# Kernel tuning notes

Measured on AMD Instinct MI355X. Metric: run time of the kernel, lower is better.

The kernel has to match this reference:

```python
import jax, jax.numpy as jnp
import numpy as np

NUM_CLASSES = 9
TEMP = 0.1
ALPHA = 0.99
EPS = 1e-12  # F.normalize default eps


def _l2norm(x, axis=-1):
    n = jnp.linalg.norm(x, axis=axis, keepdims=True)
    return x / jnp.maximum(n, EPS)


def setup_inputs() -> dict:
    key = jax.random.key(0)
    k1, k2, k3, k4, k5 = jax.random.split(key, 5)
    B, D, h, w = 4, 768, 128, 128
    return {
        "cls_score": jax.random.normal(k1, (B, NUM_CLASSES, h, w), dtype=jnp.float32),
        "label": jax.random.randint(k2, (B, 4 * h, 4 * w), 0, NUM_CLASSES, dtype=jnp.int64),
        "gt_lucas": jax.random.randint(k3, (B, 4 * h, 4 * w), 0, NUM_CLASSES, dtype=jnp.int64),
        "features": jax.random.normal(k4, (B, D, h, w), dtype=jnp.float32),
        "prototypes": jax.random.uniform(k5, (NUM_CLASSES, D), dtype=jnp.float32),
    }


def reference(cls_score, label, gt_lucas, features, prototypes):
    B, D, h, w = features.shape
    # so the masked gathers reduce to a full flatten (static shapes).
    corine = label[:, ::4, ::4].reshape(-1)          # [N]
    lucas = gt_lucas[:, ::4, ::4].reshape(-1)        # [N] (mask trivially all valid)
    feats = jnp.transpose(features, (0, 2, 3, 1)).reshape(-1, D)  # [N, D]
    N = feats.shape[0]
    # note: original indexes corine labels under the lucas mask (mask all-true here)
    labels_lucas = corine
    labels_corine = jnp.where(corine == 7, 6, corine)
    # per-class EMA prototype update (unique(labels_lucas) == arange(9) by construction;
    # compute_ema detaches the new mean)
    sums = jax.ops.segment_sum(feats, labels_lucas, num_segments=NUM_CLASSES)      # [C, D]
    counts = jax.ops.segment_sum(jnp.ones((N,), feats.dtype), labels_lucas,
                                 num_segments=NUM_CLASSES)                          # [C]
    means = jax.lax.stop_gradient(sums / counts[:, None])
    protos = ALPHA * means + (1.0 - ALPHA) * prototypes
    protos = _l2norm(protos, axis=-1)                # F.normalize over feature dim
    logits = protos @ feats.T                        # [C, N]
    prot_feat = _l2norm(logits, axis=-1) / TEMP      # normalize each class row over N
    prot_feat = prot_feat.at[2].set((labels_corine == 2).astype(prot_feat.dtype))
    E = jnp.exp(prot_feat)                           # [C, N]
    A1 = E[labels_corine, jnp.arange(N)]             # [N]
    A2 = E.sum(axis=0)                               # [N]
    return jnp.mean(-jnp.log(A1 / A2))
```

## Files before the change

### kernel.cpp

```cpp
#include <hip/hip_runtime.h>
#include <math.h>

#define NCLS 9
#define DIM 768
#define NPIX 65536

#define OFF_LAB     ((size_t)0)
#define OFF_HIST    ((size_t)65536)
#define OFF_SUMS    ((size_t)74752)
#define OFF_SUMSQ   ((size_t)102400)
#define OFF_LOSS    ((size_t)102464)
#define OFF_DONE    ((size_t)102480)
#define OFF_LOGITS  ((size_t)131072)

__device__ __forceinline__ float waveReduceSum(float v) {
#pragma unroll
  for (int off = 32; off > 0; off >>= 1) v += __shfl_down(v, off, 64);
  return v;
}

__global__ void k0_lab(const int* __restrict__ label, unsigned char* __restrict__ lab,
                       int* __restrict__ hist, float* __restrict__ sumsq,
                       float* __restrict__ lossacc, unsigned int* __restrict__ done) {
  __shared__ int h[NCLS];
  int tid = threadIdx.x;
  if (tid < NCLS) h[tid] = 0;
  __syncthreads();
  int n = blockIdx.x * 256 + tid;
  int b = n >> 14, r = (n >> 7) & 127, cc = n & 127;
  int c = label[b * 262144 + r * 2048 + cc * 4];
  lab[n] = (unsigned char)c;
  atomicAdd(&h[c], 1);
  if (blockIdx.x == 0) {
    if (tid < 16) sumsq[tid] = 0.f;
    else if (tid == 16) lossacc[0] = 0.f;
    else if (tid == 17) done[0] = 0u;
  }
  __syncthreads();
  if (tid < NCLS) hist[blockIdx.x * NCLS + tid] = h[tid];
}

__global__ void k1_segsum(const float4* __restrict__ feat4, const uchar4* __restrict__ lab4,
                          float* __restrict__ sums) {
  int d = blockIdx.x;
  int tid = threadIdx.x;
  float acc[NCLS];
#pragma unroll
  for (int k = 0; k < NCLS; ++k) acc[k] = 0.f;
  for (int b = 0; b < 4; ++b) {
    const float4* fp = feat4 + (size_t)(b * DIM + d) * 4096;
    const uchar4* lp = lab4 + b * 4096;
#pragma unroll 4
    for (int i = 0; i < 16; ++i) {
      int p = tid + i * 256;
      float4 f = fp[p];
      uchar4 l = lp[p];
      int lx = l.x, ly = l.y, lz = l.z, lw = l.w;
#pragma unroll
      for (int k = 0; k < NCLS; ++k) {
        acc[k] += (lx == k) ? f.x : 0.f;
        acc[k] += (ly == k) ? f.y : 0.f;
        acc[k] += (lz == k) ? f.z : 0.f;
        acc[k] += (lw == k) ? f.w : 0.f;
      }
    }
  }
  __shared__ float red[4][NCLS];
#pragma unroll
  for (int k = 0; k < NCLS; ++k) acc[k] = waveReduceSum(acc[k]);
  int lane = tid & 63, w = tid >> 6;
  if (lane == 0) {
#pragma unroll
    for (int k = 0; k < NCLS; ++k) red[w][k] = acc[k];
  }
  __syncthreads();
  if (tid < NCLS)
    sums[tid * DIM + d] = red[0][tid] + red[1][tid] + red[2][tid] + red[3][tid];
}

__global__ void __launch_bounds__(1024) k3_fused(const float* __restrict__ sums,
                                                 const int* __restrict__ hist,
                                                 const float* __restrict__ proto,
                                                 const float* __restrict__ feat,
                                                 float* __restrict__ logits,
                                                 float* __restrict__ sumsq) {
  __shared__ float pl[DIM * 12];
  __shared__ float cpart[32][NCLS];
  __shared__ float cnt[NCLS];
  __shared__ float red12[12][NCLS];
  __shared__ float invn[NCLS];
  __shared__ float red4[4][NCLS];
  int tid = threadIdx.x;

  if (tid < 288) {
    int c = tid % NCLS, g = tid / NCLS;
    int s = 0;
#pragma unroll
    for (int j = 0; j < 8; ++j) s += hist[(g * 8 + j) * NCLS + c];
    cpart[g][c] = (float)s;
  }
  __syncthreads();
  if (tid < NCLS) {
    float s = 0.f;
#pragma unroll
    for (int g = 0; g < 32; ++g) s += cpart[g][tid];
    cnt[tid] = s;
  }
  __syncthreads();

  float v[NCLS];
  if (tid < DIM) {
#pragma unroll
    for (int c = 0; c < NCLS; ++c)
      v[c] = 0.99f * (sums[c * DIM + tid] / cnt[c]) + 0.01f * proto[c * DIM + tid];
    int lane = tid & 63, w = tid >> 6;
#pragma unroll
    for (int c = 0; c < NCLS; ++c) {
      float q = waveReduceSum(v[c] * v[c]);
      if (lane == 0) red12[w][c] = q;
    }
  }
  __syncthreads();
  if (tid < NCLS) {
    float t = 0.f;
#pragma unroll
    for (int w2 = 0; w2 < 12; ++w2) t += red12[w2][tid];
    invn[tid] = 1.f / fmaxf(sqrtf(t), 1e-12f);
  }
  __syncthreads();
  if (tid < DIM) {
#pragma unroll
    for (int c = 0; c < NCLS; ++c) pl[tid * 12 + c] = v[c] * invn[c];
  }
  __syncthreads();

  int s = tid >> 8, p = tid & 255;
  int n = blockIdx.x * 256 + p;
  int b = n >> 14, pp = n & 16383;
  const float* fp = feat + ((size_t)(b * DIM + s * 192)) * 16384 + pp;
  const float* plbase = pl + (size_t)s * 192 * 12;
  float a0 = 0, a1 = 0, a2 = 0, a3 = 0, a4 = 0, a5 = 0, a6 = 0, a7 = 0, a8 = 0;
#pragma unroll 4
  for (int dd = 0; dd < 192; ++dd) {
    float f = fp[(size_t)dd * 16384];
    const float4* pr = (const float4*)(plbase + dd * 12);
    float4 q0 = pr[0];
    float4 q1 = pr[1];
    float q8 = plbase[dd * 12 + 8];
    a0 += q0.x * f; a1 += q0.y * f; a2 += q0.z * f; a3 += q0.w * f;
    a4 += q1.x * f; a5 += q1.y * f; a6 += q1.z * f; a7 += q1.w * f;
    a8 += q8 * f;
  }
  __syncthreads();
  if (s > 0) {
    float* rp = pl + (size_t)(s - 1) * 2304 + p * 9;
    rp[0] = a0; rp[1] = a1; rp[2] = a2; rp[3] = a3; rp[4] = a4;
    rp[5] = a5; rp[6] = a6; rp[7] = a7; rp[8] = a8;
  }
  __syncthreads();
  if (s == 0) {
#pragma unroll
    for (int q = 0; q < 3; ++q) {
      const float* rp = pl + (size_t)q * 2304 + p * 9;
      a0 += rp[0]; a1 += rp[1]; a2 += rp[2]; a3 += rp[3]; a4 += rp[4];
      a5 += rp[5]; a6 += rp[6]; a7 += rp[7]; a8 += rp[8];
    }
    float* outp = logits + n;
    outp[0 * NPIX] = a0; outp[1 * NPIX] = a1; outp[2 * NPIX] = a2;
    outp[3 * NPIX] = a3; outp[4 * NPIX] = a4; outp[5 * NPIX] = a5;
    outp[6 * NPIX] = a6; outp[7 * NPIX] = a7; outp[8 * NPIX] = a8;
    float ss[NCLS] = {a0 * a0, a1 * a1, a2 * a2, a3 * a3, a4 * a4,
                      a5 * a5, a6 * a6, a7 * a7, a8 * a8};
#pragma unroll
    for (int c = 0; c < NCLS; ++c) ss[c] = waveReduceSum(ss[c]);
    int lane = tid & 63, w = tid >> 6;
    if (lane == 0) {
#pragma unroll
      for (int c = 0; c < NCLS; ++c) red4[w][c] = ss[c];
    }
  }
  __syncthreads();
  if (tid < NCLS)
    atomicAdd(&sumsq[tid], red4[0][tid] + red4[1][tid] + red4[2][tid] + red4[3][tid]);
}

__global__ void k5_loss(const float4* __restrict__ logits4, const uchar4* __restrict__ lab4,
                        const float* __restrict__ sumsq, float* __restrict__ lossacc,
                        unsigned int* __restrict__ done, float* __restrict__ out) {
  int t = blockIdx.x * 256 + threadIdx.x;
  int tid = threadIdx.x;
  float scale[NCLS];
#pragma unroll
  for (int c = 0; c < NCLS; ++c) scale[c] = 10.f / fmaxf(sqrtf(sumsq[c]), 1e-12f);
  float arr[NCLS][4];
#pragma unroll
  for (int c = 0; c < NCLS; ++c) {
    float4 v = logits4[(size_t)c * 16384 + t];
    arr[c][0] = v.x; arr[c][1] = v.y; arr[c][2] = v.z; arr[c][3] = v.w;
  }
  uchar4 lb = lab4[t];
  int lv[4] = {lb.x, lb.y, lb.z, lb.w};
  float lsum = 0.f;
#pragma unroll
  for (int j = 0; j < 4; ++j) {
    int l = lv[j];
    int lc = (l == 7) ? 6 : l;
    float sumE = 0.f, picked = 0.f;
#pragma unroll
    for (int c = 0; c < NCLS; ++c) {
      float pf = (c == 2) ? ((lc == 2) ? 1.f : 0.f) : arr[c][j] * scale[c];
      sumE += __expf(pf);
      picked += (c == lc) ? pf : 0.f;
    }
    lsum += __logf(sumE) - picked;
  }
  lsum = waveReduceSum(lsum);
  __shared__ float red[4];
  int lane = tid & 63, w = tid >> 6;
  if (lane == 0) red[w] = lsum;
  __syncthreads();
  if (tid == 0) {
    atomicAdd(lossacc, red[0] + red[1] + red[2] + red[3]);
    __threadfence();
    unsigned int ticket = atomicAdd(done, 1u);
    if (ticket == gridDim.x - 1) {
      __threadfence();
      float total = __hip_atomic_load(lossacc, __ATOMIC_ACQUIRE, __HIP_MEMORY_SCOPE_AGENT);
      out[0] = total * (1.f / (float)NPIX);
    }
  }
}

extern "C" void kernel_launch(void* const* d_in, const int* in_sizes, int n_in,
                              void* d_out, int out_size, void* d_ws, size_t ws_size,
                              hipStream_t stream) {
  const int* label = (const int*)d_in[1];
  const float* feat = (const float*)d_in[3];
  const float* proto = (const float*)d_in[4];
  char* ws = (char*)d_ws;
  unsigned char* lab = (unsigned char*)(ws + OFF_LAB);
  int* hist = (int*)(ws + OFF_HIST);
  float* sums = (float*)(ws + OFF_SUMS);
  float* sumsq = (float*)(ws + OFF_SUMSQ);
  float* lossacc = (float*)(ws + OFF_LOSS);
  unsigned int* done = (unsigned int*)(ws + OFF_DONE);
  float* logits = (float*)(ws + OFF_LOGITS);

  k0_lab<<<NPIX / 256, 256, 0, stream>>>(label, lab, hist, sumsq, lossacc, done);
  k1_segsum<<<DIM, 256, 0, stream>>>((const float4*)feat, (const uchar4*)lab, sums);
  k3_fused<<<NPIX / 256, 1024, 0, stream>>>(sums, hist, proto, feat, logits, sumsq);
  k5_loss<<<64, 256, 0, stream>>>((const float4*)logits, (const uchar4*)lab, sumsq, lossacc,
                                  done, (float*)d_out);
}
```

Measured before the change: 98.60 us.

## Move prototype normalization to last segsum block and split D across 16 waves

The prototype EMA and L2-normalization now run once, in the last-finishing block of the segment-sum kernel via a ticket counter, and the result is written to a workspace table. Before, each of the 256 logits blocks recomputed it. The logits kernel now copies that table into shared memory and splits the feature dimension across 16 waves of 48 rows each. Each lane computes 4 pixels and 9 classes, and partial sums are combined with shared-memory atomics. This cuts redundant per-block prologue work and raises per-thread reuse of the prototype loads, at the cost of a serial tail block in segsum and contention on the LDS atomics.

```diff
diff --git a/kernel.cpp b/kernel.cpp
--- a/kernel.cpp
+++ b/kernel.cpp
@@ -11,7 +11,9 @@
 #define OFF_SUMSQ   ((size_t)102400)
 #define OFF_LOSS    ((size_t)102464)
 #define OFF_DONE    ((size_t)102480)
-#define OFF_LOGITS  ((size_t)131072)
+#define OFF_DONE1   ((size_t)102496)
+#define OFF_PROTO   ((size_t)102528)
+#define OFF_LOGITS  ((size_t)139392)
 
 __device__ __forceinline__ float waveReduceSum(float v) {
 #pragma unroll
@@ -21,7 +23,8 @@
 
 __global__ void k0_lab(const int* __restrict__ label, unsigned char* __restrict__ lab,
                        int* __restrict__ hist, float* __restrict__ sumsq,
-                       float* __restrict__ lossacc, unsigned int* __restrict__ done) {
+                       float* __restrict__ lossacc, unsigned int* __restrict__ done,
+                       unsigned int* __restrict__ done1) {
   __shared__ int h[NCLS];
   int tid = threadIdx.x;
   if (tid < NCLS) h[tid] = 0;
@@ -35,13 +38,17 @@
     if (tid < 16) sumsq[tid] = 0.f;
     else if (tid == 16) lossacc[0] = 0.f;
     else if (tid == 17) done[0] = 0u;
+    else if (tid == 18) done1[0] = 0u;
   }
   __syncthreads();
   if (tid < NCLS) hist[blockIdx.x * NCLS + tid] = h[tid];
 }
 
 __global__ void k1_segsum(const float4* __restrict__ feat4, const uchar4* __restrict__ lab4,
-                          float* __restrict__ sums) {
+                          float* __restrict__ sums, const int* __restrict__ hist,
+                          const float* __restrict__ proto, float* __restrict__ protoT,
+                          unsigned int* __restrict__ done1) {
+  __shared__ float red[4][NCLS];
   int d = blockIdx.x;
   int tid = threadIdx.x;
   float acc[NCLS];
@@ -65,7 +72,6 @@
       }
     }
   }
-  __shared__ float red[4][NCLS];
 #pragma unroll
   for (int k = 0; k < NCLS; ++k) acc[k] = waveReduceSum(acc[k]);
   int lane = tid & 63, w = tid >> 6;
@@ -76,107 +82,137 @@
   __syncthreads();
   if (tid < NCLS)
     sums[tid * DIM + d] = red[0][tid] + red[1][tid] + red[2][tid] + red[3][tid];
-}
-
-__global__ void __launch_bounds__(1024) k3_fused(const float* __restrict__ sums,
-                                                 const int* __restrict__ hist,
-                                                 const float* __restrict__ proto,
-                                                 const float* __restrict__ feat,
-                                                 float* __restrict__ logits,
-                                                 float* __restrict__ sumsq) {
-  __shared__ float pl[DIM * 12];
-  __shared__ float cpart[32][NCLS];
+
+  __threadfence();
+  __syncthreads();
+  __shared__ unsigned int tkt;
+  if (tid == 0) tkt = atomicAdd(done1, 1u);
+  __syncthreads();
+  if (tkt != gridDim.x - 1) return;
+  __threadfence();
+
+  __shared__ float cpart[16][NCLS];
   __shared__ float cnt[NCLS];
-  __shared__ float red12[12][NCLS];
   __shared__ float invn[NCLS];
-  __shared__ float red4[4][NCLS];
-  int tid = threadIdx.x;
-
-  if (tid < 288) {
+  if (tid < 144) {
     int c = tid % NCLS, g = tid / NCLS;
     int s = 0;
 #pragma unroll
-    for (int j = 0; j < 8; ++j) s += hist[(g * 8 + j) * NCLS + c];
+    for (int j = 0; j < 16; ++j) s += hist[(g * 16 + j) * NCLS + c];
     cpart[g][c] = (float)s;
   }
   __syncthreads();
   if (tid < NCLS) {
     float s = 0.f;
 #pragma unroll
-    for (int g = 0; g < 32; ++g) s += cpart[g][tid];
+    for (int g = 0; g < 16; ++g) s += cpart[g][tid];
     cnt[tid] = s;
   }
   __syncthreads();
-
-  float v[NCLS];
-  if (tid < DIM) {
+  float v[3][NCLS];
+  float q[NCLS];
+#pragma unroll
+  for (int c = 0; c < NCLS; ++c) q[c] = 0.f;
+#pragma unroll
+  for (int j = 0; j < 3; ++j) {
+    int dd = tid + j * 256;
+#pragma unroll
+    for (int c = 0; c < NCLS; ++c) {
+      float x = 0.99f * (sums[c * DIM + dd] / cnt[c]) + 0.01f * proto[c * DIM + dd];
+      v[j][c] = x;
+      q[c] += x * x;
+    }
+  }
+#pragma unroll
+  for (int c = 0; c < NCLS; ++c) q[c] = waveReduceSum(q[c]);
+  if (lane == 0) {
+#pragma unroll
+    for (int c = 0; c < NCLS; ++c) red[w][c] = q[c];
+  }
+  __syncthreads();
+  if (tid < NCLS) {
+    float t = red[0][tid] + red[1][tid] + red[2][tid] + red[3][tid];
+    invn[tid] = 1.f / fmaxf(sqrtf(t), 1e-12f);
+  }
+  __syncthreads();
+#pragma unroll
+  for (int j = 0; j < 3; ++j) {
 #pragma unroll
     for (int c = 0; c < NCLS; ++c)
-      v[c] = 0.99f * (sums[c * DIM + tid] / cnt[c]) + 0.01f * proto[c * DIM + tid];
-    int lane = tid & 63, w = tid >> 6;
-#pragma unroll
-    for (int c = 0; c < NCLS; ++c) {
-      float q = waveReduceSum(v[c] * v[c]);
-      if (lane == 0) red12[w][c] = q;
-    }
-  }
-  __syncthreads();
-  if (tid < NCLS) {
-    float t = 0.f;
-#pragma unroll
-    for (int w2 = 0; w2 < 12; ++w2) t += red12[w2][tid];
-    invn[tid] = 1.f / fmaxf(sqrtf(t), 1e-12f);
-  }
-  __syncthreads();
-  if (tid < DIM) {
-#pragma unroll
-    for (int c = 0; c < NCLS; ++c) pl[tid * 12 + c] = v[c] * invn[c];
-  }
-  __syncthreads();
-
-  int s = tid >> 8, p = tid & 255;
-  int n = blockIdx.x * 256 + p;
-  int b = n >> 14, pp = n & 16383;
-  const float* fp = feat + ((size_t)(b * DIM + s * 192)) * 16384 + pp;
-  const float* plbase = pl + (size_t)s * 192 * 12;
-  float a0 = 0, a1 = 0, a2 = 0, a3 = 0, a4 = 0, a5 = 0, a6 = 0, a7 = 0, a8 = 0;
+      protoT[(size_t)(tid + j * 256) * 12 + c] = v[j][c] * invn[c];
+  }
+}
+
+__global__ void __launch_bounds__(1024) k3_logits(const float* __restrict__ feat,
+                                                  const float* __restrict__ protoT,
+                                                  float* __restrict__ logits,
+                                                  float* __restrict__ sumsq) {
+  __shared__ float pl[DIM * 12];
+  __shared__ float accb[NCLS][256];
+  __shared__ float red4[4][NCLS];
+  int tid = threadIdx.x;
+  const float4* pt4 = (const float4*)protoT;
+  float4* pl4 = (float4*)pl;
+  float* accf = (float*)accb;
+#pragma unroll
+  for (int i = 0; i < 3; ++i) {
+    int idx = tid + i * 1024;
+    if (idx < 2304) {
+      pl4[idx] = pt4[idx];
+      accf[idx] = 0.f;
+    }
+  }
+  __syncthreads();
+
+  int s = tid >> 6, lane = tid & 63;
+  int n0 = blockIdx.x * 256;
+  int b = n0 >> 14, ppb = n0 & 16383;
+  const float* fp = feat + ((size_t)(b * DIM + s * 48)) * 16384 + ppb + lane;
+  const float* plb = pl + (size_t)s * 48 * 12;
+  float a[NCLS][4];
+#pragma unroll
+  for (int c = 0; c < NCLS; ++c)
+#pragma unroll
+    for (int j = 0; j < 4; ++j) a[c][j] = 0.f;
+
 #pragma unroll 4
-  for (int dd = 0; dd < 192; ++dd) {
-    float f = fp[(size_t)dd * 16384];
-    const float4* pr = (const float4*)(plbase + dd * 12);
+  for (int dd = 0; dd < 48; ++dd) {
+    const float* fr = fp + (size_t)dd * 16384;
+    float f[4];
+    f[0] = fr[0]; f[1] = fr[64]; f[2] = fr[128]; f[3] = fr[192];
+    const float4* pr = (const float4*)(plb + dd * 12);
     float4 q0 = pr[0];
     float4 q1 = pr[1];
-    float q8 = plbase[dd * 12 + 8];
-    a0 += q0.x * f; a1 += q0.y * f; a2 += q0.z * f; a3 += q0.w * f;
-    a4 += q1.x * f; a5 += q1.y * f; a6 += q1.z * f; a7 += q1.w * f;
-    a8 += q8 * f;
-  }
-  __syncthreads();
-  if (s > 0) {
-    float* rp = pl + (size_t)(s - 1) * 2304 + p * 9;
-    rp[0] = a0; rp[1] = a1; rp[2] = a2; rp[3] = a3; rp[4] = a4;
-    rp[5] = a5; rp[6] = a6; rp[7] = a7; rp[8] = a8;
-  }
-  __syncthreads();
-  if (s == 0) {
-#pragma unroll
-    for (int q = 0; q < 3; ++q) {
-      const float* rp = pl + (size_t)q * 2304 + p * 9;
-      a0 += rp[0]; a1 += rp[1]; a2 += rp[2]; a3 += rp[3]; a4 += rp[4];
-      a5 += rp[5]; a6 += rp[6]; a7 += rp[7]; a8 += rp[8];
-    }
-    float* outp = logits + n;
-    outp[0 * NPIX] = a0; outp[1 * NPIX] = a1; outp[2 * NPIX] = a2;
-    outp[3 * NPIX] = a3; outp[4 * NPIX] = a4; outp[5 * NPIX] = a5;
-    outp[6 * NPIX] = a6; outp[7 * NPIX] = a7; outp[8 * NPIX] = a8;
-    float ss[NCLS] = {a0 * a0, a1 * a1, a2 * a2, a3 * a3, a4 * a4,
-                      a5 * a5, a6 * a6, a7 * a7, a8 * a8};
+    float q8 = plb[dd * 12 + 8];
+    float pcs[NCLS] = {q0.x, q0.y, q0.z, q0.w, q1.x, q1.y, q1.z, q1.w, q8};
+#pragma unroll
+    for (int c = 0; c < NCLS; ++c)
+#pragma unroll
+      for (int j = 0; j < 4; ++j) a[c][j] += pcs[c] * f[j];
+  }
+
+#pragma unroll
+  for (int c = 0; c < NCLS; ++c)
+#pragma unroll
+    for (int j = 0; j < 4; ++j)
+      atomicAdd(&accb[c][lane + 64 * j], a[c][j]);
+  __syncthreads();
+
+  if (tid < 256) {
+    int n = n0 + tid;
+    float ss[NCLS];
+#pragma unroll
+    for (int c = 0; c < NCLS; ++c) {
+      float vv = accb[c][tid];
+      logits[(size_t)c * NPIX + n] = vv;
+      ss[c] = vv * vv;
+    }
 #pragma unroll
     for (int c = 0; c < NCLS; ++c) ss[c] = waveReduceSum(ss[c]);
-    int lane = tid & 63, w = tid >> 6;
-    if (lane == 0) {
-#pragma unroll
-      for (int c = 0; c < NCLS; ++c) red4[w][c] = ss[c];
+    int l2 = tid & 63, w2 = tid >> 6;
+    if (l2 == 0) {
+#pragma unroll
+      for (int c = 0; c < NCLS; ++c) red4[w2][c] = ss[c];
     }
   }
   __syncthreads();
@@ -244,11 +280,14 @@
   float* sumsq = (float*)(ws + OFF_SUMSQ);
   float* lossacc = (float*)(ws + OFF_LOSS);
   unsigned int* done = (unsigned int*)(ws + OFF_DONE);
+  unsigned int* done1 = (unsigned int*)(ws + OFF_DONE1);
+  float* protoT = (float*)(ws + OFF_PROTO);
   float* logits = (float*)(ws + OFF_LOGITS);
 
-  k0_lab<<<NPIX / 256, 256, 0, stream>>>(label, lab, hist, sumsq, lossacc, done);
-  k1_segsum<<<DIM, 256, 0, stream>>>((const float4*)feat, (const uchar4*)lab, sums);
-  k3_fused<<<NPIX / 256, 1024, 0, stream>>>(sums, hist, proto, feat, logits, sumsq);
+  k0_lab<<<NPIX / 256, 256, 0, stream>>>(label, lab, hist, sumsq, lossacc, done, done1);
+  k1_segsum<<<DIM, 256, 0, stream>>>((const float4*)feat, (const uchar4*)lab, sums, hist,
+                                     proto, protoT, done1);
+  k3_logits<<<NPIX / 256, 1024, 0, stream>>>(feat, protoT, logits, sumsq);
   k5_loss<<<64, 256, 0, stream>>>((const float4*)logits, (const uchar4*)lab, sumsq, lossacc,
                                   done, (float*)d_out);
 }
```

After: 205.3 us. 2.08x slower.

## Fuse logits and loss kernels with grid-wide barrier, keep logits in registers

Applied to the files above, without the earlier changes.

Merges the projection kernel and the loss kernel into one launch. Each block publishes per-class partial sums of squares, waits at a software grid barrier (atomic counter plus spin), then reduces all partials and computes the loss straight from register-held logits. This removes the global logits buffer write and read-back and one kernel launch. The barrier only works if all 256 blocks of 1024 threads are co-resident, and spinning adds latency.

```diff
diff --git a/kernel.cpp b/kernel.cpp
--- a/kernel.cpp
+++ b/kernel.cpp
@@ -8,10 +8,9 @@
 #define OFF_LAB     ((size_t)0)
 #define OFF_HIST    ((size_t)65536)
 #define OFF_SUMS    ((size_t)74752)
-#define OFF_SUMSQ   ((size_t)102400)
-#define OFF_LOSS    ((size_t)102464)
-#define OFF_DONE    ((size_t)102480)
-#define OFF_LOGITS  ((size_t)131072)
+#define OFF_SSQP    ((size_t)102400)
+#define OFF_LOSS    ((size_t)111616)
+#define OFF_DONE    ((size_t)111632)
 
 __device__ __forceinline__ float waveReduceSum(float v) {
 #pragma unroll
@@ -20,8 +19,8 @@
 }
 
 __global__ void k0_lab(const int* __restrict__ label, unsigned char* __restrict__ lab,
-                       int* __restrict__ hist, float* __restrict__ sumsq,
-                       float* __restrict__ lossacc, unsigned int* __restrict__ done) {
+                       int* __restrict__ hist, float* __restrict__ lossacc,
+                       unsigned int* __restrict__ done) {
   __shared__ int h[NCLS];
   int tid = threadIdx.x;
   if (tid < NCLS) h[tid] = 0;
@@ -32,9 +31,9 @@
   lab[n] = (unsigned char)c;
   atomicAdd(&h[c], 1);
   if (blockIdx.x == 0) {
-    if (tid < 16) sumsq[tid] = 0.f;
-    else if (tid == 16) lossacc[0] = 0.f;
+    if (tid == 16) lossacc[0] = 0.f;
     else if (tid == 17) done[0] = 0u;
+    else if (tid == 18) done[1] = 0u;
   }
   __syncthreads();
   if (tid < NCLS) hist[blockIdx.x * NCLS + tid] = h[tid];
@@ -78,18 +77,20 @@
     sums[tid * DIM + d] = red[0][tid] + red[1][tid] + red[2][tid] + red[3][tid];
 }
 
-__global__ void __launch_bounds__(1024) k3_fused(const float* __restrict__ sums,
-                                                 const int* __restrict__ hist,
-                                                 const float* __restrict__ proto,
-                                                 const float* __restrict__ feat,
-                                                 float* __restrict__ logits,
-                                                 float* __restrict__ sumsq) {
+__global__ void __launch_bounds__(1024, 4) k3_mega(
+    const float* __restrict__ sums, const int* __restrict__ hist,
+    const float* __restrict__ proto, const float* __restrict__ feat,
+    const unsigned char* __restrict__ lab, float* __restrict__ ssqpart,
+    float* __restrict__ lossacc, unsigned int* __restrict__ done,
+    float* __restrict__ out) {
   __shared__ float pl[DIM * 12];
   __shared__ float cpart[32][NCLS];
   __shared__ float cnt[NCLS];
   __shared__ float red12[12][NCLS];
   __shared__ float invn[NCLS];
   __shared__ float red4[4][NCLS];
+  __shared__ float scale_s[NCLS];
+  __shared__ float lred[4];
   int tid = threadIdx.x;
 
   if (tid < 288) {
@@ -108,45 +109,46 @@
   }
   __syncthreads();
 
-  float v[NCLS];
-  if (tid < DIM) {
-#pragma unroll
-    for (int c = 0; c < NCLS; ++c)
-      v[c] = 0.99f * (sums[c * DIM + tid] / cnt[c]) + 0.01f * proto[c * DIM + tid];
-    int lane = tid & 63, w = tid >> 6;
-#pragma unroll
-    for (int c = 0; c < NCLS; ++c) {
-      float q = waveReduceSum(v[c] * v[c]);
-      if (lane == 0) red12[w][c] = q;
-    }
-  }
-  __syncthreads();
-  if (tid < NCLS) {
-    float t = 0.f;
-#pragma unroll
-    for (int w2 = 0; w2 < 12; ++w2) t += red12[w2][tid];
-    invn[tid] = 1.f / fmaxf(sqrtf(t), 1e-12f);
-  }
-  __syncthreads();
-  if (tid < DIM) {
-#pragma unroll
-    for (int c = 0; c < NCLS; ++c) pl[tid * 12 + c] = v[c] * invn[c];
-  }
-  __syncthreads();
+  {
+    float v[NCLS];
+    if (tid < DIM) {
+#pragma unroll
+      for (int c = 0; c < NCLS; ++c)
+        v[c] = 0.99f * (sums[c * DIM + tid] / cnt[c]) + 0.01f * proto[c * DIM + tid];
+      int lane = tid & 63, w = tid >> 6;
+#pragma unroll
+      for (int c = 0; c < NCLS; ++c) {
+        float q = waveReduceSum(v[c] * v[c]);
+        if (lane == 0) red12[w][c] = q;
+      }
+    }
+    __syncthreads();
+    if (tid < NCLS) {
+      float t = 0.f;
+#pragma unroll
+      for (int w2 = 0; w2 < 12; ++w2) t += red12[w2][tid];
+      invn[tid] = 1.f / fmaxf(sqrtf(t), 1e-12f);
+    }
+    __syncthreads();
+    if (tid < DIM) {
+#pragma unroll
+      for (int c = 0; c < NCLS; ++c) pl[tid * 12 + c] = v[c] * invn[c];
+    }
+    __syncthreads();
+  }
 
   int s = tid >> 8, p = tid & 255;
   int n = blockIdx.x * 256 + p;
   int b = n >> 14, pp = n & 16383;
   const float* fp = feat + ((size_t)(b * DIM + s * 192)) * 16384 + pp;
-  const float* plbase = pl + (size_t)s * 192 * 12;
   float a0 = 0, a1 = 0, a2 = 0, a3 = 0, a4 = 0, a5 = 0, a6 = 0, a7 = 0, a8 = 0;
 #pragma unroll 4
   for (int dd = 0; dd < 192; ++dd) {
     float f = fp[(size_t)dd * 16384];
-    const float4* pr = (const float4*)(plbase + dd * 12);
+    const float4* pr = (const float4*)&pl[(s * 192 + dd) * 12];
     float4 q0 = pr[0];
     float4 q1 = pr[1];
-    float q8 = plbase[dd * 12 + 8];
+    float q8 = pl[(s * 192 + dd) * 12 + 8];
     a0 += q0.x * f; a1 += q0.y * f; a2 += q0.z * f; a3 += q0.w * f;
     a4 += q1.x * f; a5 += q1.y * f; a6 += q1.z * f; a7 += q1.w * f;
     a8 += q8 * f;
@@ -165,10 +167,6 @@
       a0 += rp[0]; a1 += rp[1]; a2 += rp[2]; a3 += rp[3]; a4 += rp[4];
       a5 += rp[5]; a6 += rp[6]; a7 += rp[7]; a8 += rp[8];
     }
-    float* outp = logits + n;
-    outp[0 * NPIX] = a0; outp[1 * NPIX] = a1; outp[2 * NPIX] = a2;
-    outp[3 * NPIX] = a3; outp[4 * NPIX] = a4; outp[5 * NPIX] = a5;
-    outp[6 * NPIX] = a6; outp[7 * NPIX] = a7; outp[8 * NPIX] = a8;
     float ss[NCLS] = {a0 * a0, a1 * a1, a2 * a2, a3 * a3, a4 * a4,
                       a5 * a5, a6 * a6, a7 * a7, a8 * a8};
 #pragma unroll
@@ -180,49 +178,62 @@
     }
   }
   __syncthreads();
-  if (tid < NCLS)
-    atomicAdd(&sumsq[tid], red4[0][tid] + red4[1][tid] + red4[2][tid] + red4[3][tid]);
-}
-
-__global__ void k5_loss(const float4* __restrict__ logits4, const uchar4* __restrict__ lab4,
-                        const float* __restrict__ sumsq, float* __restrict__ lossacc,
-                        unsigned int* __restrict__ done, float* __restrict__ out) {
-  int t = blockIdx.x * 256 + threadIdx.x;
-  int tid = threadIdx.x;
-  float scale[NCLS];
-#pragma unroll
-  for (int c = 0; c < NCLS; ++c) scale[c] = 10.f / fmaxf(sqrtf(sumsq[c]), 1e-12f);
-  float arr[NCLS][4];
-#pragma unroll
-  for (int c = 0; c < NCLS; ++c) {
-    float4 v = logits4[(size_t)c * 16384 + t];
-    arr[c][0] = v.x; arr[c][1] = v.y; arr[c][2] = v.z; arr[c][3] = v.w;
-  }
-  uchar4 lb = lab4[t];
-  int lv[4] = {lb.x, lb.y, lb.z, lb.w};
-  float lsum = 0.f;
-#pragma unroll
-  for (int j = 0; j < 4; ++j) {
-    int l = lv[j];
+  if (tid < NCLS) {
+    float t = red4[0][tid] + red4[1][tid] + red4[2][tid] + red4[3][tid];
+    __hip_atomic_store(&ssqpart[blockIdx.x * NCLS + tid], t, __ATOMIC_RELAXED,
+                       __HIP_MEMORY_SCOPE_AGENT);
+  }
+  __syncthreads();
+
+  if (tid == 0) {
+    __threadfence();
+    atomicAdd(&done[0], 1u);
+    while (__hip_atomic_load(&done[0], __ATOMIC_ACQUIRE, __HIP_MEMORY_SCOPE_AGENT) <
+           gridDim.x) {
+      __builtin_amdgcn_s_sleep(2);
+    }
+  }
+  __syncthreads();
+
+  if (tid < 288) {
+    int c = tid % NCLS, g = tid / NCLS;
+    float t = 0.f;
+#pragma unroll
+    for (int j = 0; j < 8; ++j)
+      t += __hip_atomic_load(&ssqpart[(g * 8 + j) * NCLS + c], __ATOMIC_RELAXED,
+                             __HIP_MEMORY_SCOPE_AGENT);
+    cpart[g][c] = t;
+  }
+  __syncthreads();
+  if (tid < NCLS) {
+    float t = 0.f;
+#pragma unroll
+    for (int g = 0; g < 32; ++g) t += cpart[g][tid];
+    scale_s[tid] = 10.f / fmaxf(sqrtf(t), 1e-12f);
+  }
+  __syncthreads();
+
+  if (s == 0) {
+    int l = lab[n];
     int lc = (l == 7) ? 6 : l;
+    float av[NCLS] = {a0, a1, a2, a3, a4, a5, a6, a7, a8};
     float sumE = 0.f, picked = 0.f;
 #pragma unroll
     for (int c = 0; c < NCLS; ++c) {
-      float pf = (c == 2) ? ((lc == 2) ? 1.f : 0.f) : arr[c][j] * scale[c];
+      float pf = (c == 2) ? ((lc == 2) ? 1.f : 0.f) : av[c] * scale_s[c];
       sumE += __expf(pf);
       picked += (c == lc) ? pf : 0.f;
     }
-    lsum += __logf(sumE) - picked;
-  }
-  lsum = waveReduceSum(lsum);
-  __shared__ float red[4];
-  int lane = tid & 63, w = tid >> 6;
-  if (lane == 0) red[w] = lsum;
+    float lsum = __logf(sumE) - picked;
+    lsum = waveReduceSum(lsum);
+    int lane = tid & 63, w = tid >> 6;
+    if (lane == 0) lred[w] = lsum;
+  }
   __syncthreads();
   if (tid == 0) {
-    atomicAdd(lossacc, red[0] + red[1] + red[2] + red[3]);
+    atomicAdd(lossacc, lred[0] + lred[1] + lred[2] + lred[3]);
     __threadfence();
-    unsigned int ticket = atomicAdd(done, 1u);
+    unsigned int ticket = atomicAdd(&done[1], 1u);
     if (ticket == gridDim.x - 1) {
       __threadfence();
       float total = __hip_atomic_load(lossacc, __ATOMIC_ACQUIRE, __HIP_MEMORY_SCOPE_AGENT);
@@ -241,14 +252,12 @@
   unsigned char* lab = (unsigned char*)(ws + OFF_LAB);
   int* hist = (int*)(ws + OFF_HIST);
   float* sums = (float*)(ws + OFF_SUMS);
-  float* sumsq = (float*)(ws + OFF_SUMSQ);
+  float* ssqpart = (float*)(ws + OFF_SSQP);
   float* lossacc = (float*)(ws + OFF_LOSS);
   unsigned int* done = (unsigned int*)(ws + OFF_DONE);
-  float* logits = (float*)(ws + OFF_LOGITS);
-
-  k0_lab<<<NPIX / 256, 256, 0, stream>>>(label, lab, hist, sumsq, lossacc, done);
+
+  k0_lab<<<NPIX / 256, 256, 0, stream>>>(label, lab, hist, lossacc, done);
   k1_segsum<<<DIM, 256, 0, stream>>>((const float4*)feat, (const uchar4*)lab, sums);
-  k3_fused<<<NPIX / 256, 1024, 0, stream>>>(sums, hist, proto, feat, logits, sumsq);
-  k5_loss<<<64, 256, 0, stream>>>((const float4*)logits, (const uchar4*)lab, sumsq, lossacc,
-                                  done, (float*)d_out);
-}
+  k3_mega<<<NPIX / 256, 1024, 0, stream>>>(sums, hist, proto, feat, lab, ssqpart,
+                                           lossacc, done, (float*)d_out);
+}
```

Measured after the change: 122.2 us. +24.0%, slower.
